# Kernel optimization log

Measured on AMD Instinct MI355X. Metric: run time of the kernel, lower is better.

Reference implementation:

```python
import jax, jax.numpy as jnp
import numpy as np
import math

DIM_MODEL = 1024
N_HEAD = 16
NUM_NEURON = 64
MAX_LEN = 2048
B, S = 4, 2048


def setup_inputs() -> dict:
    key = jax.random.key(0)
    ks = jax.random.split(key, 11)
    d, p = DIM_MODEL, N_HEAD * NUM_NEURON
    sc_in = 1.0 / math.sqrt(d)
    sc_p = 1.0 / math.sqrt(p)
    return {
        "q": jax.random.normal(ks[0], (B, S, d), jnp.float32),
        "k": jax.random.normal(ks[1], (B, S, d), jnp.float32),
        "v": jax.random.normal(ks[2], (B, S, d), jnp.float32),
        "Wq": jax.random.normal(ks[3], (d, p), jnp.float32) * sc_in,
        "bq": jnp.zeros((p,), jnp.float32),
        "Wk": jax.random.normal(ks[4], (d, p), jnp.float32) * sc_in,
        "bk": jnp.zeros((p,), jnp.float32),
        "Wv": jax.random.normal(ks[5], (d, p), jnp.float32) * sc_in,
        "bv": jnp.zeros((p,), jnp.float32),
        "Wf": jax.random.normal(ks[6], (p, d), jnp.float32) * sc_p,
        "bf": jnp.zeros((d,), jnp.float32),
    }


def _split_heads(x):  # [B,S,H*Dh] -> [B,H,S,Dh]
    b, s, _ = x.shape
    return x.reshape(b, s, N_HEAD, NUM_NEURON).transpose(0, 2, 1, 3)


def reference(q, k, v, Wq, bq, Wk, bk, Wv, bv, Wf, bf):
    qh = _split_heads(q @ Wq + bq)
    kh = _split_heads(k @ Wk + bk)
    vh = _split_heads(v @ Wv + bv)
    # NOTE: original scales by 1/sqrt(max_len), not 1/sqrt(head_dim)
    scores = jnp.einsum("bhqd,bhkd->bhqk", qh, kh) / math.sqrt(MAX_LEN)
    s = scores.shape[-1]
    causal = jnp.tril(jnp.ones((s, s), bool))  # [S,S]
    scores = jnp.where(causal[None, None], scores, -jnp.inf)
    attn = jax.nn.softmax(scores, axis=-1)
    out = jnp.einsum("bhqk,bhkd->bhqd", attn, vh)  # [B,H,S,Dh]
    c = out.transpose(0, 2, 1, 3).reshape(out.shape[0], out.shape[2], N_HEAD * NUM_NEURON)
    return c @ Wf + bf
```

## Files before the change

kernel.cpp:

```cpp
#include <hip/hip_runtime.h>
#include <stdint.h>

#define DMODEL 1024
#define NHEAD 16
#define DH 64
#define BB 4
#define SS 2048
#define MROWS (BB * SS)

typedef __bf16 bfx8 __attribute__((ext_vector_type(8)));
typedef float f32x4 __attribute__((ext_vector_type(4)));
typedef float fvec4 __attribute__((ext_vector_type(4)));
typedef int i32x4 __attribute__((ext_vector_type(4)));
typedef unsigned short u16x8 __attribute__((ext_vector_type(8)));
typedef unsigned short u16x4 __attribute__((ext_vector_type(4)));

__device__ __forceinline__ unsigned short f2bf(float f) {
    union { float f; unsigned int u; } v; v.f = f;
    unsigned int r = v.u + 0x7FFFu + ((v.u >> 16) & 1u);
    return (unsigned short)(r >> 16);
}

__device__ __forceinline__ unsigned int cvtpk(float lo, float hi) {
    unsigned int r;
    asm("v_cvt_pk_bf16_f32 %0, %1, %2" : "=v"(r) : "v"(lo), "v"(hi));
    return r;
}

typedef __attribute__((address_space(1))) const void gas_t;
typedef __attribute__((address_space(3))) void las_t;
__device__ __forceinline__ void gload_lds16(const void* g, void* l) {
    __builtin_amdgcn_global_load_lds((gas_t*)g, (las_t*)l, 16, 0, 0);
}

__device__ __forceinline__ int sigma_k(int i) {
    return (i & 0x20) | ((i & 0x0C) << 1) | ((i & 0x10) >> 2) | (i & 3);
}

__global__ void transpose_cvt4_kernel(const float* __restrict__ W0, unsigned short* __restrict__ T0,
                                      const float* __restrict__ W1, unsigned short* __restrict__ T1,
                                      const float* __restrict__ W2, unsigned short* __restrict__ T2,
                                      const float* __restrict__ W3, unsigned short* __restrict__ T3)
{
    const float* W = (blockIdx.z == 0) ? W0 : (blockIdx.z == 1) ? W1
                   : (blockIdx.z == 2) ? W2 : W3;
    unsigned short* Wt = (blockIdx.z == 0) ? T0 : (blockIdx.z == 1) ? T1
                       : (blockIdx.z == 2) ? T2 : T3;
    __shared__ unsigned short t[64][72];
    const int tid = threadIdx.x;
    const int r0 = blockIdx.y * 64, c0 = blockIdx.x * 64;
    #pragma unroll
    for (int i = 0; i < 4; ++i) {
        int idx = tid + i * 256;
        int r = idx >> 4, c4 = idx & 15;
        fvec4 v = *reinterpret_cast<const fvec4*>(&W[(size_t)(r0 + r) * DMODEL + c0 + c4 * 4]);
        #pragma unroll
        for (int j = 0; j < 4; ++j) t[c4 * 4 + j][r] = f2bf(v[j]);
    }
    __syncthreads();
    #pragma unroll
    for (int i = 0; i < 2; ++i) {
        int idx = tid + i * 256;
        int r = idx >> 3, c8 = idx & 7;
        u16x8 v = *reinterpret_cast<const u16x8*>(&t[r][c8 * 8]);
        *reinterpret_cast<u16x8*>(&Wt[(size_t)(c0 + r) * DMODEL + r0 + c8 * 8]) = v;
    }
}

struct GArg {
    const void* A;
    const unsigned short* Bt;
    const float* bias;
    void* O;
    float osc;
    int mode;
};

template<bool A_FP32>
__global__ __launch_bounds__(256, A_FP32 ? 3 : 4)
void gemm_kernel(GArg g0, GArg g1, GArg g2, int M, int N, int K)
{
    const GArg g = (blockIdx.z == 0) ? g0 : (blockIdx.z == 1) ? g1 : g2;
    __shared__ unsigned short sA[128 * 64];
    __shared__ unsigned short sB[128 * 64];
    const int tid  = threadIdx.x;
    const int lane = tid & 63;
    const int wave = tid >> 6;
    const int wm = (wave >> 1) * 64, wn = (wave & 1) * 64;
    const int m0 = blockIdx.x * 128, n0 = blockIdx.y * 128;
    const int lr = lane & 15;
    const int lg = lane >> 4;
    const int arow = tid >> 3, acol8 = tid & 7;

    f32x4 acc[4][4] = {};
    fvec4 ar[4][2];

    if constexpr (A_FP32) {
        const float* Af = (const float*)g.A;
        #pragma unroll
        for (int i = 0; i < 4; ++i) {
            const float* src = &Af[(size_t)(m0 + arow + i * 32) * K + acol8 * 8];
            ar[i][0] = *reinterpret_cast<const fvec4*>(src);
            ar[i][1] = *reinterpret_cast<const fvec4*>(src + 4);
        }
    }

    for (int kk0 = 0; kk0 < K; kk0 += 64) {
        __syncthreads();
        if constexpr (A_FP32) {
            #pragma unroll
            for (int i = 0; i < 4; ++i) {
                union { i32x4 i4; u16x8 u; } pk;
                pk.i4[0] = cvtpk(ar[i][0][0], ar[i][0][1]);
                pk.i4[1] = cvtpk(ar[i][0][2], ar[i][0][3]);
                pk.i4[2] = cvtpk(ar[i][1][0], ar[i][1][1]);
                pk.i4[3] = cvtpk(ar[i][1][2], ar[i][1][3]);
                *reinterpret_cast<u16x8*>(&sA[(arow + i * 32) * 64 + acol8 * 8]) = pk.u;
            }
            #pragma unroll
            for (int i = 0; i < 4; ++i) {
                int c = tid + i * 256;
                int row = c >> 3, col8 = c & 7;
                gload_lds16(&g.Bt[(size_t)(n0 + row) * K + kk0 + col8 * 8], &sB[c * 8]);
            }
            __builtin_amdgcn_sched_barrier(0);
            const bool more = (kk0 + 64 < K);
            if (more) {
                const float* Af = (const float*)g.A;
                #pragma unroll
                for (int i = 0; i < 4; ++i) {
                    const float* src = &Af[(size_t)(m0 + arow + i * 32) * K + kk0 + 64 + acol8 * 8];
                    ar[i][0] = *reinterpret_cast<const fvec4*>(src);
                    ar[i][1] = *reinterpret_cast<const fvec4*>(src + 4);
                }
            }
            __builtin_amdgcn_sched_barrier(0);
            if (more) asm volatile("s_waitcnt vmcnt(8) lgkmcnt(0)" ::: "memory");
            else      asm volatile("s_waitcnt vmcnt(0) lgkmcnt(0)" ::: "memory");
            __builtin_amdgcn_sched_barrier(0);
            __builtin_amdgcn_s_barrier();
            __builtin_amdgcn_sched_barrier(0);
        } else {
            #pragma unroll
            for (int i = 0; i < 4; ++i) {
                int c = tid + i * 256;
                int row = c >> 3, col8 = c & 7;
                gload_lds16(&((const unsigned short*)g.A)[(size_t)(m0 + row) * K + kk0 + col8 * 8],
                            &sA[c * 8]);
            }
            #pragma unroll
            for (int i = 0; i < 4; ++i) {
                int c = tid + i * 256;
                int row = c >> 3, col8 = c & 7;
                gload_lds16(&g.Bt[(size_t)(n0 + row) * K + kk0 + col8 * 8], &sB[c * 8]);
            }
            __syncthreads();
        }

        #pragma unroll
        for (int kk = 0; kk < 2; ++kk) {
            bfx8 af[4], bfr[4];
            #pragma unroll
            for (int m = 0; m < 4; ++m)
                af[m] = *reinterpret_cast<const bfx8*>(
                    &sA[(wm + m * 16 + lr) * 64 + kk * 32 + lg * 8]);
            #pragma unroll
            for (int n = 0; n < 4; ++n)
                bfr[n] = *reinterpret_cast<const bfx8*>(
                    &sB[(wn + n * 16 + lr) * 64 + kk * 32 + lg * 8]);
            #pragma unroll
            for (int m = 0; m < 4; ++m)
                #pragma unroll
                for (int n = 0; n < 4; ++n)
                    acc[m][n] = __builtin_amdgcn_mfma_f32_16x16x32_bf16(
                        af[m], bfr[n], acc[m][n], 0, 0, 0);
        }
    }

    #pragma unroll
    for (int n = 0; n < 4; ++n) {
        int col = n0 + wn + n * 16 + lr;
        float bv = g.bias[col];
        #pragma unroll
        for (int m = 0; m < 4; ++m) {
            int rowb = m0 + wm + m * 16 + lg * 4;
            float val[4];
            #pragma unroll
            for (int r = 0; r < 4; ++r) val[r] = (acc[m][n][r] + bv) * g.osc;
            if (g.mode == 0) {
                #pragma unroll
                for (int r = 0; r < 4; ++r)
                    ((unsigned short*)g.O)[(size_t)(rowb + r) * N + col] = f2bf(val[r]);
            } else if (g.mode == 2) {
                #pragma unroll
                for (int r = 0; r < 4; ++r)
                    ((float*)g.O)[(size_t)(rowb + r) * N + col] = val[r];
            } else {
                int bq = rowb >> 11, s = rowb & 2047;
                int hh = col >> 6, d = col & 63;
                u16x4 pk;
                #pragma unroll
                for (int r = 0; r < 4; ++r) pk[r] = f2bf(val[r]);
                size_t idx = ((size_t)(bq * 16 + hh) * 64 + d) * 2048 + s;
                *reinterpret_cast<u16x4*>(&((unsigned short*)g.O)[idx]) = pk;
            }
        }
    }
}

__global__ __launch_bounds__(512, 4)
void attn_kernel(const unsigned short* __restrict__ Q,
                 const unsigned short* __restrict__ K,
                 const unsigned short* __restrict__ Vt,
                 unsigned short* __restrict__ C)
{
    __shared__ unsigned short sK[2][8192];
    __shared__ unsigned short sV[2][8192];

    const int tid  = threadIdx.x;
    const int lane = tid & 63;
    const int wave = tid >> 6;
    const int lr = lane & 15, lg = lane >> 4;
    const int bh = blockIdx.x;
    const int p  = blockIdx.y;
    const int b = bh >> 4, h = bh & 15;
    const size_t rowbase = (size_t)b * SS;
    const int hcol = h * DH;

    const int srow = tid >> 3, sc8 = tid & 7;
    const int sig  = sigma_k(srow);
    const int woff = srow * 64 + ((sc8 ^ (srow & 7)) * 8);
    const int p0 = lg ^ (lr & 7);

    const u16x8 onesu = {0x3F80, 0x3F80, 0x3F80, 0x3F80, 0x3F80, 0x3F80, 0x3F80, 0x3F80};
    union { u16x8 u; bfx8 b; } onesc; onesc.u = onesu;
    const bfx8 ones = onesc.b;

    #pragma unroll
    for (int ph = 0; ph < 2; ++ph) {
        const int qt = ph ? p : (15 - p);
        const int q0 = qt * 128;

        bfx8 aq[2];
        {
            int qr = q0 + wave * 16 + lr;
            const unsigned short* qp = &Q[(rowbase + qr) * DMODEL + hcol + lg * 8];
            aq[0] = *reinterpret_cast<const bfx8*>(qp);
            aq[1] = *reinterpret_cast<const bfx8*>(qp + 32);
        }

        float m_run = 0.f;
        f32x4 acc_l = {};
        f32x4 acc_o[4] = {};
        bool mz = true;
        const int qmax_wave = q0 + wave * 16 + 15;
        const int npairs = qt + 1;

        u16x8 rk[2], rv[2];
        #pragma unroll
        for (int s = 0; s < 2; ++s) {
            rk[s] = *reinterpret_cast<const u16x8*>(
                &K[(rowbase + s * 64 + sig) * DMODEL + hcol + sc8 * 8]);
            rv[s] = *reinterpret_cast<const u16x8*>(
                &Vt[((size_t)bh * DH + srow) * SS + s * 64 + sc8 * 8]);
        }
        #pragma unroll
        for (int s = 0; s < 2; ++s) {
            *reinterpret_cast<u16x8*>(&sK[0][s * 4096 + woff]) = rk[s];
            *reinterpret_cast<u16x8*>(&sV[0][s * 4096 + woff]) = rv[s];
        }
        if (npairs > 1) {
            #pragma unroll
            for (int s = 0; s < 2; ++s) {
                const int kk = (2 + s) * 64;
                rk[s] = *reinterpret_cast<const u16x8*>(
                    &K[(rowbase + kk + sig) * DMODEL + hcol + sc8 * 8]);
                rv[s] = *reinterpret_cast<const u16x8*>(
                    &Vt[((size_t)bh * DH + srow) * SS + kk + sc8 * 8]);
            }
        }
        __syncthreads();

        for (int u = 0; u < npairs; ++u) {
            const int cur = u & 1;
            #pragma unroll
            for (int s = 0; s < 2; ++s) {
                const int k0 = (2 * u + s) * 64;
                if (k0 > qmax_wave) break;

                f32x4 sc[4];
                __builtin_amdgcn_s_setprio(1);
                #pragma unroll
                for (int nf = 0; nf < 4; ++nf) {
                    int i = nf * 16 + lr;
                    bfx8 ak0 = *reinterpret_cast<const bfx8*>(&sK[cur][s * 4096 + i * 64 + p0 * 8]);
                    bfx8 ak1 = *reinterpret_cast<const bfx8*>(&sK[cur][s * 4096 + i * 64 + (p0 ^ 4) * 8]);
                    f32x4 sv = {0.f, 0.f, 0.f, 0.f};
                    sv = __builtin_amdgcn_mfma_f32_16x16x32_bf16(ak0, aq[0], sv, 0, 0, 0);
                    sv = __builtin_amdgcn_mfma_f32_16x16x32_bf16(ak1, aq[1], sv, 0, 0, 0);
                    sc[nf] = sv;
                }
                __builtin_amdgcn_s_setprio(0);
                if (k0 + 63 > q0 + wave * 16) {
                    int qrow = q0 + wave * 16 + lr;
                    #pragma unroll
                    for (int nf = 0; nf < 4; ++nf) {
                        int kb = k0 + ((nf >> 1) << 5) + (lg << 3) + ((nf & 1) << 2);
                        #pragma unroll
                        for (int r = 0; r < 4; ++r)
                            if (kb + r > qrow) sc[nf][r] = -3.0e38f;
                    }
                }
                float a0 = fmaxf(fmaxf(sc[0][0], sc[0][1]), sc[0][2]);
                float a1 = fmaxf(fmaxf(sc[0][3], sc[1][0]), sc[1][1]);
                float a2 = fmaxf(fmaxf(sc[1][2], sc[1][3]), sc[2][0]);
                float a3 = fmaxf(fmaxf(sc[2][1], sc[2][2]), sc[2][3]);
                float a4 = fmaxf(fmaxf(sc[3][0], sc[3][1]), sc[3][2]);
                float pmax = fmaxf(fmaxf(fmaxf(a0, a1), fmaxf(a2, a3)),
                                   fmaxf(a4, sc[3][3]));
                if (mz && __all(pmax <= 8.0f)) {
                    #pragma unroll
                    for (int nf = 0; nf < 4; ++nf)
                        #pragma unroll
                        for (int r = 0; r < 4; ++r)
                            sc[nf][r] = __builtin_exp2f(sc[nf][r]);
                } else {
                    mz = false;
                    float mx = pmax;
                    mx = fmaxf(mx, __shfl_xor(mx, 16, 64));
                    mx = fmaxf(mx, __shfl_xor(mx, 32, 64));
                    float mnew = fmaxf(m_run, mx);
                    float fs = __builtin_exp2f(m_run - mnew);
                    m_run = mnew;
                    #pragma unroll
                    for (int nf = 0; nf < 4; ++nf)
                        #pragma unroll
                        for (int r = 0; r < 4; ++r)
                            sc[nf][r] = __builtin_exp2f(sc[nf][r] - mnew);
                    #pragma unroll
                    for (int r = 0; r < 4; ++r) {
                        float fsa = __shfl(fs, lg * 4 + r, 64);
                        #pragma unroll
                        for (int d = 0; d < 4; ++d) acc_o[d][r] *= fsa;
                        acc_l[r] *= fsa;
                    }
                }
                #pragma unroll
                for (int h2 = 0; h2 < 2; ++h2) {
                    union { i32x4 i; bfx8 b; } pa;
                    pa.i[0] = cvtpk(sc[2 * h2][0],     sc[2 * h2][1]);
                    pa.i[1] = cvtpk(sc[2 * h2][2],     sc[2 * h2][3]);
                    pa.i[2] = cvtpk(sc[2 * h2 + 1][0], sc[2 * h2 + 1][1]);
                    pa.i[3] = cvtpk(sc[2 * h2 + 1][2], sc[2 * h2 + 1][3]);
                    __builtin_amdgcn_s_setprio(1);
                    acc_l = __builtin_amdgcn_mfma_f32_16x16x32_bf16(pa.b, ones, acc_l, 0, 0, 0);
                    #pragma unroll
                    for (int d = 0; d < 4; ++d) {
                        int i = d * 16 + lr;
                        int pv = ((h2 << 2) | lg) ^ (lr & 7);
                        bfx8 bv0 = *reinterpret_cast<const bfx8*>(&sV[cur][s * 4096 + i * 64 + pv * 8]);
                        acc_o[d] = __builtin_amdgcn_mfma_f32_16x16x32_bf16(pa.b, bv0, acc_o[d], 0, 0, 0);
                    }
                    __builtin_amdgcn_s_setprio(0);
                }
            }
            if (u + 1 < npairs) {
                #pragma unroll
                for (int s = 0; s < 2; ++s) {
                    *reinterpret_cast<u16x8*>(&sK[cur ^ 1][s * 4096 + woff]) = rk[s];
                    *reinterpret_cast<u16x8*>(&sV[cur ^ 1][s * 4096 + woff]) = rv[s];
                }
                if (u + 2 < npairs) {
                    #pragma unroll
                    for (int s = 0; s < 2; ++s) {
                        const int kk = (2 * u + 4 + s) * 64;
                        rk[s] = *reinterpret_cast<const u16x8*>(
                            &K[(rowbase + kk + sig) * DMODEL + hcol + sc8 * 8]);
                        rv[s] = *reinterpret_cast<const u16x8*>(
                            &Vt[((size_t)bh * DH + srow) * SS + kk + sc8 * 8]);
                    }
                }
            }
            __syncthreads();
        }

        f32x4 linv;
        #pragma unroll
        for (int r = 0; r < 4; ++r) linv[r] = 1.0f / acc_l[r];
        const int qrb = q0 + wave * 16 + lg * 4;
        #pragma unroll
        for (int d = 0; d < 4; ++d) {
            int col = hcol + d * 16 + lr;
            #pragma unroll
            for (int r = 0; r < 4; ++r)
                C[(rowbase + qrb + r) * DMODEL + col] = f2bf(acc_o[d][r] * linv[r]);
        }
    }
}

extern "C" void kernel_launch(void* const* d_in, const int* in_sizes, int n_in,
                              void* d_out, int out_size, void* d_ws, size_t ws_size,
                              hipStream_t stream)
{
    const float* q  = (const float*)d_in[0];
    const float* k  = (const float*)d_in[1];
    const float* v  = (const float*)d_in[2];
    const float* Wq = (const float*)d_in[3];
    const float* bq = (const float*)d_in[4];
    const float* Wk = (const float*)d_in[5];
    const float* bk = (const float*)d_in[6];
    const float* Wv = (const float*)d_in[7];
    const float* bv = (const float*)d_in[8];
    const float* Wf = (const float*)d_in[9];
    const float* bf = (const float*)d_in[10];

    unsigned short* ws = (unsigned short*)d_ws;
    const size_t SZ = (size_t)MROWS * DMODEL;
    unsigned short* Vt = ws;
    unsigned short* Cb = ws + SZ;
    unsigned short* Kb = ws + 3 * SZ;

    unsigned short* scr = (unsigned short*)d_out;
    unsigned short* WqT = scr;
    unsigned short* WkT = scr + 1048576;
    unsigned short* WvT = scr + 2097152;
    unsigned short* WfT = scr + 3145728;
    unsigned short* Qb  = scr + 4194304;

    const float qscale = 0.02209708691207961f * 1.44269504088896341f;

    transpose_cvt4_kernel<<<dim3(16, 16, 4), 256, 0, stream>>>(
        Wq, WqT, Wk, WkT, Wv, WvT, Wf, WfT);

    {
        GArg gq{q, WqT, bq, Qb, qscale, 0};
        GArg gk{k, WkT, bk, Kb, 1.0f,   0};
        GArg gv{v, WvT, bv, Vt, 1.0f,   3};
        gemm_kernel<true><<<dim3(64, 8, 3), 256, 0, stream>>>(
            gq, gk, gv, MROWS, DMODEL, DMODEL);
    }

    attn_kernel<<<dim3(BB * NHEAD, 8), 512, 0, stream>>>(Qb, Kb, Vt, Cb);

    {
        GArg gf{Cb, WfT, bf, (float*)d_out, 1.0f, 2};
        gemm_kernel<false><<<dim3(64, 8, 1), 256, 0, stream>>>(
            gf, gf, gf, MROWS, DMODEL, DMODEL);
    }
}
```

Before: 180.2 us.

## Double-buffer B tile in LDS for fp32-A GEMM path

```diff
diff --git a/kernel.cpp b/kernel.cpp
--- a/kernel.cpp
+++ b/kernel.cpp
@@ -82,7 +82,7 @@
 {
     const GArg g = (blockIdx.z == 0) ? g0 : (blockIdx.z == 1) ? g1 : g2;
     __shared__ unsigned short sA[128 * 64];
-    __shared__ unsigned short sB[128 * 64];
+    __shared__ unsigned short sB[(A_FP32 ? 2 : 1) * 128 * 64];
     const int tid  = threadIdx.x;
     const int lane = tid & 63;
     const int wave = tid >> 6;
@@ -96,6 +96,13 @@
     fvec4 ar[4][2];
 
     if constexpr (A_FP32) {
+        #pragma unroll
+        for (int i = 0; i < 4; ++i) {
+            int c = tid + i * 256;
+            int row = c >> 3, col8 = c & 7;
+            gload_lds16(&g.Bt[(size_t)(n0 + row) * K + col8 * 8], &sB[c * 8]);
+        }
+        __builtin_amdgcn_sched_barrier(0);
         const float* Af = (const float*)g.A;
         #pragma unroll
         for (int i = 0; i < 4; ++i) {
@@ -103,11 +110,16 @@
             ar[i][0] = *reinterpret_cast<const fvec4*>(src);
             ar[i][1] = *reinterpret_cast<const fvec4*>(src + 4);
         }
+        __builtin_amdgcn_sched_barrier(0);
     }
 
     for (int kk0 = 0; kk0 < K; kk0 += 64) {
-        __syncthreads();
         if constexpr (A_FP32) {
+            const int cur = (kk0 >> 6) & 1;
+            const bool more = (kk0 + 64 < K);
+            __builtin_amdgcn_sched_barrier(0);
+            __builtin_amdgcn_s_barrier();
+            __builtin_amdgcn_sched_barrier(0);
             #pragma unroll
             for (int i = 0; i < 4; ++i) {
                 union { i32x4 i4; u16x8 u; } pk;
@@ -117,14 +129,17 @@
                 pk.i4[3] = cvtpk(ar[i][1][2], ar[i][1][3]);
                 *reinterpret_cast<u16x8*>(&sA[(arow + i * 32) * 64 + acol8 * 8]) = pk.u;
             }
-            #pragma unroll
-            for (int i = 0; i < 4; ++i) {
-                int c = tid + i * 256;
-                int row = c >> 3, col8 = c & 7;
-                gload_lds16(&g.Bt[(size_t)(n0 + row) * K + kk0 + col8 * 8], &sB[c * 8]);
-            }
-            __builtin_amdgcn_sched_barrier(0);
-            const bool more = (kk0 + 64 < K);
+            __builtin_amdgcn_sched_barrier(0);
+            if (more) {
+                #pragma unroll
+                for (int i = 0; i < 4; ++i) {
+                    int c = tid + i * 256;
+                    int row = c >> 3, col8 = c & 7;
+                    gload_lds16(&g.Bt[(size_t)(n0 + row) * K + kk0 + 64 + col8 * 8],
+                                &sB[(cur ^ 1) * 8192 + c * 8]);
+                }
+            }
+            __builtin_amdgcn_sched_barrier(0);
             if (more) {
                 const float* Af = (const float*)g.A;
                 #pragma unroll
@@ -135,12 +150,32 @@
                 }
             }
             __builtin_amdgcn_sched_barrier(0);
-            if (more) asm volatile("s_waitcnt vmcnt(8) lgkmcnt(0)" ::: "memory");
-            else      asm volatile("s_waitcnt vmcnt(0) lgkmcnt(0)" ::: "memory");
+            asm volatile("s_waitcnt lgkmcnt(0)" ::: "memory");
             __builtin_amdgcn_sched_barrier(0);
             __builtin_amdgcn_s_barrier();
             __builtin_amdgcn_sched_barrier(0);
+
+            const unsigned short* sBc = &sB[cur * 8192];
+            #pragma unroll
+            for (int kk = 0; kk < 2; ++kk) {
+                bfx8 af[4], bfr[4];
+                #pragma unroll
+                for (int m = 0; m < 4; ++m)
+                    af[m] = *reinterpret_cast<const bfx8*>(
+                        &sA[(wm + m * 16 + lr) * 64 + kk * 32 + lg * 8]);
+                #pragma unroll
+                for (int n = 0; n < 4; ++n)
+                    bfr[n] = *reinterpret_cast<const bfx8*>(
+                        &sBc[(wn + n * 16 + lr) * 64 + kk * 32 + lg * 8]);
+                #pragma unroll
+                for (int m = 0; m < 4; ++m)
+                    #pragma unroll
+                    for (int n = 0; n < 4; ++n)
+                        acc[m][n] = __builtin_amdgcn_mfma_f32_16x16x32_bf16(
+                            af[m], bfr[n], acc[m][n], 0, 0, 0);
+            }
         } else {
+            __syncthreads();
             #pragma unroll
             for (int i = 0; i < 4; ++i) {
                 int c = tid + i * 256;
@@ -155,25 +190,25 @@
                 gload_lds16(&g.Bt[(size_t)(n0 + row) * K + kk0 + col8 * 8], &sB[c * 8]);
             }
             __syncthreads();
-        }
-
-        #pragma unroll
-        for (int kk = 0; kk < 2; ++kk) {
-            bfx8 af[4], bfr[4];
-            #pragma unroll
-            for (int m = 0; m < 4; ++m)
-                af[m] = *reinterpret_cast<const bfx8*>(
-                    &sA[(wm + m * 16 + lr) * 64 + kk * 32 + lg * 8]);
-            #pragma unroll
-            for (int n = 0; n < 4; ++n)
-                bfr[n] = *reinterpret_cast<const bfx8*>(
-                    &sB[(wn + n * 16 + lr) * 64 + kk * 32 + lg * 8]);
-            #pragma unroll
-            for (int m = 0; m < 4; ++m)
+
+            #pragma unroll
+            for (int kk = 0; kk < 2; ++kk) {
+                bfx8 af[4], bfr[4];
+                #pragma unroll
+                for (int m = 0; m < 4; ++m)
+                    af[m] = *reinterpret_cast<const bfx8*>(
+                        &sA[(wm + m * 16 + lr) * 64 + kk * 32 + lg * 8]);
                 #pragma unroll
                 for (int n = 0; n < 4; ++n)
-                    acc[m][n] = __builtin_amdgcn_mfma_f32_16x16x32_bf16(
-                        af[m], bfr[n], acc[m][n], 0, 0, 0);
+                    bfr[n] = *reinterpret_cast<const bfx8*>(
+                        &sB[(wn + n * 16 + lr) * 64 + kk * 32 + lg * 8]);
+                #pragma unroll
+                for (int m = 0; m < 4; ++m)
+                    #pragma unroll
+                    for (int n = 0; n < 4; ++n)
+                        acc[m][n] = __builtin_amdgcn_mfma_f32_16x16x32_bf16(
+                            af[m], bfr[n], acc[m][n], 0, 0, 0);
+            }
         }
     }
 
```

New measurement: 178.6 us, median of 2. About the same (-0.9%).
